# Kernel optimization log

Measured on AMD Instinct MI355X. Metric: run time of the kernel, lower is better.

## Reference

```python
import jax, jax.numpy as jnp
import numpy as np

B, T, E = 4, 2048, 1024
HS = 64            # attention_head_size
NH = E // HS       # num_heads = 16 (all heads share one weight set in the original)


def setup_inputs() -> dict:
    key = jax.random.key(0)
    ks = jax.random.split(key, 6)
    s = 0.02
    x = jax.random.normal(ks[0], (B, T, E), dtype=jnp.float32)
    Wq = jax.random.normal(ks[1], (E, HS), dtype=jnp.float32) * s
    Wk = jax.random.normal(ks[2], (E, HS), dtype=jnp.float32) * s
    Wv = jax.random.normal(ks[3], (E, HS), dtype=jnp.float32) * s
    Wp = jax.random.normal(ks[4], (E, E), dtype=jnp.float32) * s
    bp = jax.random.normal(ks[5], (E,), dtype=jnp.float32) * s
    return {"x": x, "Wq": Wq, "Wk": Wk, "Wv": Wv, "Wp": Wp, "bp": bp}


def reference(x, Wq, Wk, Wv, Wp, bp):
    # Single shared head (the torch module replicates one Head instance NH times).
    hs = Wq.shape[1]
    num_heads = Wp.shape[0] // hs
    q = jnp.einsum('bte,eh->bth', x, Wq)   # [B,T,HS]
    k = jnp.einsum('bte,eh->bth', x, Wk)
    v = jnp.einsum('bte,eh->bth', x, Wv)
    att = jnp.einsum('bqh,bkh->bqk', q, k) * (hs ** -0.5)  # [B,T,T]
    t = x.shape[1]
    causal = jnp.tril(jnp.ones((t, t), dtype=bool))
    att = jnp.where(causal, att, jnp.finfo(att.dtype).min)
    att = jax.nn.softmax(att, axis=-1)
    head = jnp.einsum('bqk,bkh->bqh', att, v)              # [B,T,HS]
    # Concat of identical head outputs == tile along feature dim.
    out = jnp.tile(head, (1, 1, num_heads))                # [B,T,E]
    out = jnp.einsum('bte,ef->btf', out, Wp) + bp          # output projection
    return out
```

## Files before the change

### kernel.cpp

```cpp
#include <hip/hip_runtime.h>
#include <hip/hip_bf16.h>

#define T_SEQ 2048
#define E_DIM 1024
#define HSZ   64
#define NBAT  4
#define QB    64
#define NQT   32

typedef __attribute__((ext_vector_type(8))) short short8;
typedef __attribute__((ext_vector_type(4))) float f32x4;

__device__ inline short f2bf(float f) {
  union { float f; unsigned u; } v; v.f = f;
  unsigned r = v.u + 0x7FFFu + ((v.u >> 16) & 1u);
  return (short)(r >> 16);
}

__global__ __launch_bounds__(256) void wpr_kernel(const float* __restrict__ Wp,
                                                  float* __restrict__ Wpr) {
  int idx = blockIdx.x * 256 + threadIdx.x;
  int f = idx & (E_DIM - 1);
  int j = idx >> 10;
  float s = 0.f;
#pragma unroll
  for (int h = 0; h < 16; ++h) s += Wp[(size_t)(h * HSZ + j) * E_DIM + f];
  Wpr[idx] = s;
}

__global__ __launch_bounds__(256) void wt_kernel(const float* __restrict__ Wq,
    const float* __restrict__ Wk, const float* __restrict__ Wv,
    short* __restrict__ Wt) {
  int idx = blockIdx.x * 256 + threadIdx.x;
  int kk = idx & 63;
  int tmp = idx >> 6;
  int kt = tmp / 192;
  int n = tmp - kt * 192;
  const float* W = (n < 64) ? Wq : (n < 128) ? Wk : Wv;
  Wt[idx] = f2bf(W[(size_t)(kt * 64 + kk) * HSZ + (n & 63)]);
}

__global__ __launch_bounds__(256) void qkv_mfma(const float* __restrict__ X,
    const short* __restrict__ Wt, short* __restrict__ Qo,
    short* __restrict__ Ko, short* __restrict__ Vt) {
  __shared__ short Xs[16 * 64];
  __shared__ short Ws[192 * 64];

  const int tid = threadIdx.x;
  const int m0 = blockIdx.x * 16;
  const int lane = tid & 63, w = tid >> 6;
  const int l15 = lane & 15, l4 = lane >> 4;

  f32x4 acc[3];
  acc[0] = (f32x4)0.f; acc[1] = (f32x4)0.f; acc[2] = (f32x4)0.f;

  for (int kt = 0; kt < 16; ++kt) {
    const int k0 = kt * 64;
    if (tid < 128) {
      int r = tid >> 3, c = tid & 7;
      const float* s = &X[(size_t)(m0 + r) * E_DIM + k0 + c * 8];
      float4 a = *(const float4*)s, d = *(const float4*)(s + 4);
      short8 f;
      f[0] = f2bf(a.x); f[1] = f2bf(a.y); f[2] = f2bf(a.z); f[3] = f2bf(a.w);
      f[4] = f2bf(d.x); f[5] = f2bf(d.y); f[6] = f2bf(d.z); f[7] = f2bf(d.w);
      *(short8*)&Xs[r * 64 + ((c ^ (r & 7)) * 8)] = f;
    }
    {
      const short* wsrc = Wt + (size_t)kt * 12288;
#pragma unroll
      for (int i = 0; i < 6; ++i) {
        int ci = tid + i * 256;
        int r = ci >> 3, c = ci & 7;
        short8 f = *(const short8*)&wsrc[ci * 8];
        *(short8*)&Ws[r * 64 + ((c ^ (r & 7)) * 8)] = f;
      }
    }
    __syncthreads();
#pragma unroll
    for (int ks = 0; ks < 2; ++ks) {
      short8 af = *(short8*)&Xs[l15 * 64 + (((ks * 4 + l4) ^ (l15 & 7)) * 8)];
#pragma unroll
      for (int i = 0; i < 3; ++i) {
        int n = (w * 3 + i) * 16 + l15;
        short8 bf = *(short8*)&Ws[n * 64 + (((ks * 4 + l4) ^ (n & 7)) * 8)];
        acc[i] = __builtin_amdgcn_mfma_f32_16x16x32_bf16(af, bf, acc[i], 0, 0, 0);
      }
    }
    __syncthreads();
  }

  const int b = m0 >> 11, t = m0 & 2047;
#pragma unroll
  for (int i = 0; i < 3; ++i) {
    const int nb = w * 3 + i;
    const int col = (nb & 3) * 16 + l15;
    const int sel = nb >> 2;
#pragma unroll
    for (int reg = 0; reg < 4; ++reg) {
      const int row = l4 * 4 + reg;
      short v = f2bf(acc[i][reg]);
      if (sel == 0)      Qo[(size_t)(m0 + row) * HSZ + col] = v;
      else if (sel == 1) Ko[(size_t)(m0 + row) * HSZ + col] = v;
      else               Vt[((size_t)b * HSZ + col) * T_SEQ + t + row] = v;
    }
  }
}

__global__ __launch_bounds__(256) void attn_part(const short* __restrict__ Q,
    const short* __restrict__ K, const short* __restrict__ Vt,
    float* __restrict__ Opart, float* __restrict__ mpart,
    float* __restrict__ lpart, int splits) {
  const int qt = blockIdx.x;
  const int sp = blockIdx.y;
  const int b  = blockIdx.z;
  const int ntile = qt + 1;
  const int t0 = (sp * ntile) / splits;
  const int t1 = ((sp + 1) * ntile) / splits;
  const int q0 = qt * QB;
  const int pidx = (b * NQT + qt) * splits + sp;
  float* Op = Opart + (size_t)pidx * QB * HSZ;
  float* mp = mpart + (size_t)pidx * QB;
  float* lp = lpart + (size_t)pidx * QB;
  const int tid = threadIdx.x;

  if (t0 >= t1) {
    if (tid < QB) { mp[tid] = -1e30f; lp[tid] = 0.f; }
    return;
  }

  const short* Qb  = Q  + (size_t)b * T_SEQ * HSZ;
  const short* Kb  = K  + (size_t)b * T_SEQ * HSZ;
  const short* Vtb = Vt + (size_t)b * HSZ * T_SEQ;

  __shared__ short Ks[64 * 64];
  __shared__ short Vs[64 * 64];
  __shared__ short Ps[4][16 * 64];

  const int lane = tid & 63;
  const int w    = tid >> 6;
  const int l15  = lane & 15;
  const int l4   = lane >> 4;

  short8 qf[2];
#pragma unroll
  for (int ks = 0; ks < 2; ++ks)
    qf[ks] = *(const short8*)&Qb[(size_t)(q0 + w * 16 + l15) * HSZ + ks * 32 + l4 * 8];

  f32x4 o[4];
  float m_[4], l_[4];
#pragma unroll
  for (int i = 0; i < 4; ++i) { o[i] = (f32x4)0.f; m_[i] = -1e30f; l_[i] = 0.f; }

  for (int kt = t0; kt < t1; ++kt) {
    const int kv0 = kt * 64;
#pragma unroll
    for (int ci = tid; ci < 512; ci += 256) {
      int r = ci >> 3, c = ci & 7;
      short8 f = *(const short8*)&Kb[(size_t)(kv0 + r) * HSZ + c * 8];
      *(short8*)&Ks[r * 64 + ((c ^ (r & 7)) * 8)] = f;
    }
#pragma unroll
    for (int ci = tid; ci < 512; ci += 256) {
      int r = ci >> 3, c = ci & 7;
      short8 f = *(const short8*)&Vtb[(size_t)r * T_SEQ + kv0 + c * 8];
      *(short8*)&Vs[r * 64 + ((c ^ (r & 7)) * 8)] = f;
    }
    __syncthreads();

    f32x4 sacc[4];
#pragma unroll
    for (int nb = 0; nb < 4; ++nb) sacc[nb] = (f32x4)0.f;
#pragma unroll
    for (int nb = 0; nb < 4; ++nb) {
      const int krow = nb * 16 + l15;
#pragma unroll
      for (int ks = 0; ks < 2; ++ks) {
        short8 kf = *(short8*)&Ks[krow * 64 + (((ks * 4 + l4) ^ (krow & 7)) * 8)];
        sacc[nb] = __builtin_amdgcn_mfma_f32_16x16x32_bf16(qf[ks], kf, sacc[nb],
                                                           0, 0, 0);
      }
    }

    const bool diag = (kt == qt);
#pragma unroll
    for (int reg = 0; reg < 4; ++reg) {
      const int grow = q0 + w * 16 + l4 * 4 + reg;
      float sv[4];
      float rmax = -1e30f;
#pragma unroll
      for (int nb = 0; nb < 4; ++nb) {
        sv[nb] = sacc[nb][reg] * 0.125f;
        if (diag && (kv0 + nb * 16 + l15 > grow)) sv[nb] = -1e30f;
        rmax = fmaxf(rmax, sv[nb]);
      }
#pragma unroll
      for (int d = 1; d < 16; d <<= 1) rmax = fmaxf(rmax, __shfl_xor(rmax, d));
      const float mn = fmaxf(m_[reg], rmax);
      const float sc = __expf(m_[reg] - mn);
      float rsum = 0.f;
#pragma unroll
      for (int nb = 0; nb < 4; ++nb) {
        sv[nb] = __expf(sv[nb] - mn);
        rsum += sv[nb];
      }
#pragma unroll
      for (int d = 1; d < 16; d <<= 1) rsum += __shfl_xor(rsum, d);
      l_[reg] = l_[reg] * sc + rsum;
      m_[reg] = mn;
#pragma unroll
      for (int hb = 0; hb < 4; ++hb) o[hb][reg] *= sc;
      const int prow = l4 * 4 + reg;
#pragma unroll
      for (int nb = 0; nb < 4; ++nb) {
        const int col = nb * 16 + l15;
        Ps[w][prow * 64 + (((col >> 3) ^ (prow & 7)) * 8) + (col & 7)] =
            f2bf(sv[nb]);
      }
    }

#pragma unroll
    for (int ks = 0; ks < 2; ++ks) {
      const int prow = l15;
      short8 pf = *(short8*)&Ps[w][prow * 64 + (((ks * 4 + l4) ^ (prow & 7)) * 8)];
#pragma unroll
      for (int hb = 0; hb < 4; ++hb) {
        const int vrow = hb * 16 + l15;
        short8 vf = *(short8*)&Vs[vrow * 64 + (((ks * 4 + l4) ^ (vrow & 7)) * 8)];
        o[hb] = __builtin_amdgcn_mfma_f32_16x16x32_bf16(pf, vf, o[hb], 0, 0, 0);
      }
    }
    __syncthreads();
  }

#pragma unroll
  for (int hb = 0; hb < 4; ++hb)
#pragma unroll
    for (int reg = 0; reg < 4; ++reg)
      Op[(size_t)(w * 16 + l4 * 4 + reg) * HSZ + hb * 16 + l15] = o[hb][reg];
  if (l15 == 0) {
#pragma unroll
    for (int reg = 0; reg < 4; ++reg) {
      mp[w * 16 + l4 * 4 + reg] = m_[reg];
      lp[w * 16 + l4 * 4 + reg] = l_[reg];
    }
  }
}

__global__ __launch_bounds__(256) void attn_combine(
    const float* __restrict__ Opart, const float* __restrict__ mpart,
    const float* __restrict__ lpart, float* __restrict__ Hd, int splits) {
  const int qt = blockIdx.x, b = blockIdx.y;
  const int row = threadIdx.x >> 2;
  const int c0 = (threadIdx.x & 3) * 16;
  const int pbase = (b * NQT + qt) * splits;

  float M = -1e30f;
  for (int s = 0; s < splits; ++s)
    M = fmaxf(M, mpart[(size_t)(pbase + s) * QB + row]);

  float L = 0.f;
  float acc[16];
#pragma unroll
  for (int c = 0; c < 16; ++c) acc[c] = 0.f;

  for (int s = 0; s < splits; ++s) {
    const float ms = mpart[(size_t)(pbase + s) * QB + row];
    const float ls = lpart[(size_t)(pbase + s) * QB + row];
    const float w = __expf(ms - M);
    L += w * ls;
    const float* Op = Opart + ((size_t)(pbase + s) * QB + row) * HSZ + c0;
#pragma unroll
    for (int cc = 0; cc < 16; cc += 4) {
      float4 v = *(const float4*)&Op[cc];
      acc[cc + 0] += w * v.x; acc[cc + 1] += w * v.y;
      acc[cc + 2] += w * v.z; acc[cc + 3] += w * v.w;
    }
  }

  const float inv = 1.f / L;
  float* dst = Hd + ((size_t)b * T_SEQ + qt * QB + row) * HSZ + c0;
#pragma unroll
  for (int cc = 0; cc < 16; cc += 4) {
    float4 v = make_float4(acc[cc] * inv, acc[cc + 1] * inv,
                           acc[cc + 2] * inv, acc[cc + 3] * inv);
    *(float4*)&dst[cc] = v;
  }
}

__global__ __launch_bounds__(256) void proj_kernel(const float* __restrict__ Hd,
    const float* __restrict__ Wpr, const float* __restrict__ bp,
    float* __restrict__ Out) {
  __shared__ float Ht[64][68];
  __shared__ float Ws[64][132];
  const int tid = threadIdx.x;
  const int row0 = blockIdx.x * 64;
  const int c0 = blockIdx.y * 128;

  {
    int c = tid & 15, r0 = tid >> 4;
#pragma unroll
    for (int it = 0; it < 4; ++it) {
      int r = r0 + it * 16;
      float4 hv = *(const float4*)&Hd[(size_t)(row0 + r) * HSZ + c * 4];
      Ht[c * 4 + 0][r] = hv.x; Ht[c * 4 + 1][r] = hv.y;
      Ht[c * 4 + 2][r] = hv.z; Ht[c * 4 + 3][r] = hv.w;
    }
  }
  {
    int c = tid & 31, r0 = tid >> 5;
#pragma unroll
    for (int it = 0; it < 8; ++it) {
      int r = r0 + it * 8;
      *(float4*)&Ws[r][c * 4] =
          *(const float4*)&Wpr[(size_t)r * E_DIM + c0 + c * 4];
    }
  }
  __syncthreads();

  const int tx = tid & 15, ty = tid >> 4;
  float acc[4][8] = {};
#pragma unroll
  for (int k = 0; k < 64; ++k) {
    float4 a = *(const float4*)&Ht[k][ty * 4];
    float4 b0 = *(const float4*)&Ws[k][tx * 8];
    float4 b1 = *(const float4*)&Ws[k][tx * 8 + 4];
    float av[4] = {a.x, a.y, a.z, a.w};
    float bv[8] = {b0.x, b0.y, b0.z, b0.w, b1.x, b1.y, b1.z, b1.w};
#pragma unroll
    for (int i = 0; i < 4; ++i)
#pragma unroll
      for (int j = 0; j < 8; ++j) acc[i][j] += av[i] * bv[j];
  }

#pragma unroll
  for (int i = 0; i < 4; ++i) {
    const int row = row0 + ty * 4 + i;
    float4 v0, v1;
    v0.x = acc[i][0] + bp[c0 + tx * 8 + 0];
    v0.y = acc[i][1] + bp[c0 + tx * 8 + 1];
    v0.z = acc[i][2] + bp[c0 + tx * 8 + 2];
    v0.w = acc[i][3] + bp[c0 + tx * 8 + 3];
    v1.x = acc[i][4] + bp[c0 + tx * 8 + 4];
    v1.y = acc[i][5] + bp[c0 + tx * 8 + 5];
    v1.z = acc[i][6] + bp[c0 + tx * 8 + 6];
    v1.w = acc[i][7] + bp[c0 + tx * 8 + 7];
    *(float4*)&Out[(size_t)row * E_DIM + c0 + tx * 8] = v0;
    *(float4*)&Out[(size_t)row * E_DIM + c0 + tx * 8 + 4] = v1;
  }
}

extern "C" void kernel_launch(void* const* d_in, const int* in_sizes, int n_in,
                              void* d_out, int out_size, void* d_ws,
                              size_t ws_size, hipStream_t stream) {
  (void)in_sizes; (void)n_in; (void)out_size;
  const float* x  = (const float*)d_in[0];
  const float* Wq = (const float*)d_in[1];
  const float* Wk = (const float*)d_in[2];
  const float* Wv = (const float*)d_in[3];
  const float* Wp = (const float*)d_in[4];
  const float* bp = (const float*)d_in[5];
  float* out = (float*)d_out;

  float* ws   = (float*)d_ws;
  short* Qb16 = (short*)(ws);
  short* Kb16 = (short*)(ws + 262144);
  short* Vt16 = (short*)(ws + 524288);
  float* Hd   = ws + 786432;
  float* Wpr  = ws + 1310720;
  short* Wt   = (short*)(ws + 1376256);
  const size_t base = 1474560;

  int splits = 8;
  const size_t per_split = (size_t)NBAT * NQT * (QB * HSZ + 2 * QB);
  while (splits > 1 && (base + per_split * splits) * 4 > ws_size) splits >>= 1;

  float* Opart = ws + base;
  float* mpart = Opart + (size_t)NBAT * NQT * splits * QB * HSZ;
  float* lpart = mpart + (size_t)NBAT * NQT * splits * QB;

  wpr_kernel<<<dim3(256), dim3(256), 0, stream>>>(Wp, Wpr);
  wt_kernel<<<dim3(768), dim3(256), 0, stream>>>(Wq, Wk, Wv, Wt);
  qkv_mfma<<<dim3(512), dim3(256), 0, stream>>>(x, Wt, Qb16, Kb16, Vt16);
  attn_part<<<dim3(NQT, splits, NBAT), dim3(256), 0, stream>>>(
      Qb16, Kb16, Vt16, Opart, mpart, lpart, splits);
  attn_combine<<<dim3(NQT, NBAT), dim3(256), 0, stream>>>(
      Opart, mpart, lpart, Hd, splits);
  proj_kernel<<<dim3(128, 8), dim3(256), 0, stream>>>(Hd, Wpr, bp, out);
}
```

Before: 157.6 us.

## Run output projection on bf16 MFMA with transposed bf16 reduced weights

The output projection moves from an fp32 FMA GEMM staged through shared memory to a bf16 MFMA kernel. It reads the head output and the head-summed projection weights directly from global memory as bf16 fragments. The combine kernel now writes the head output as bf16, and the weight-reduction kernel writes a transposed bf16 copy. This halves intermediate traffic and uses matrix cores, at the cost of bf16 rounding of the head output and weights. The output stores are scalar and strided by row, which may limit write coalescing.

New measurement: 150.3 us. 4.7% less time.

```diff
diff --git a/kernel.cpp b/kernel.cpp
--- a/kernel.cpp
+++ b/kernel.cpp
@@ -18,14 +18,14 @@
 }
 
 __global__ __launch_bounds__(256) void wpr_kernel(const float* __restrict__ Wp,
-                                                  float* __restrict__ Wpr) {
+                                                  short* __restrict__ Wpb) {
   int idx = blockIdx.x * 256 + threadIdx.x;
   int f = idx & (E_DIM - 1);
   int j = idx >> 10;
   float s = 0.f;
 #pragma unroll
   for (int h = 0; h < 16; ++h) s += Wp[(size_t)(h * HSZ + j) * E_DIM + f];
-  Wpr[idx] = s;
+  Wpb[(size_t)f * HSZ + j] = f2bf(s);
 }
 
 __global__ __launch_bounds__(256) void wt_kernel(const float* __restrict__ Wq,
@@ -248,7 +248,7 @@
 
 __global__ __launch_bounds__(256) void attn_combine(
     const float* __restrict__ Opart, const float* __restrict__ mpart,
-    const float* __restrict__ lpart, float* __restrict__ Hd, int splits) {
+    const float* __restrict__ lpart, short* __restrict__ Hd16, int splits) {
   const int qt = blockIdx.x, b = blockIdx.y;
   const int row = threadIdx.x >> 2;
   const int c0 = (threadIdx.x & 3) * 16;
@@ -278,74 +278,43 @@
   }
 
   const float inv = 1.f / L;
-  float* dst = Hd + ((size_t)b * T_SEQ + qt * QB + row) * HSZ + c0;
-#pragma unroll
-  for (int cc = 0; cc < 16; cc += 4) {
-    float4 v = make_float4(acc[cc] * inv, acc[cc + 1] * inv,
-                           acc[cc + 2] * inv, acc[cc + 3] * inv);
-    *(float4*)&dst[cc] = v;
-  }
-}
-
-__global__ __launch_bounds__(256) void proj_kernel(const float* __restrict__ Hd,
-    const float* __restrict__ Wpr, const float* __restrict__ bp,
+  short* dst = Hd16 + ((size_t)b * T_SEQ + qt * QB + row) * HSZ + c0;
+  short8 v0, v1;
+#pragma unroll
+  for (int cc = 0; cc < 8; ++cc) {
+    v0[cc] = f2bf(acc[cc] * inv);
+    v1[cc] = f2bf(acc[8 + cc] * inv);
+  }
+  *(short8*)dst = v0;
+  *(short8*)(dst + 8) = v1;
+}
+
+__global__ __launch_bounds__(256) void proj_mfma(const short* __restrict__ Hd16,
+    const short* __restrict__ Wpb, const float* __restrict__ bp,
     float* __restrict__ Out) {
-  __shared__ float Ht[64][68];
-  __shared__ float Ws[64][132];
   const int tid = threadIdx.x;
-  const int row0 = blockIdx.x * 64;
-  const int c0 = blockIdx.y * 128;
-
-  {
-    int c = tid & 15, r0 = tid >> 4;
-#pragma unroll
-    for (int it = 0; it < 4; ++it) {
-      int r = r0 + it * 16;
-      float4 hv = *(const float4*)&Hd[(size_t)(row0 + r) * HSZ + c * 4];
-      Ht[c * 4 + 0][r] = hv.x; Ht[c * 4 + 1][r] = hv.y;
-      Ht[c * 4 + 2][r] = hv.z; Ht[c * 4 + 3][r] = hv.w;
-    }
-  }
-  {
-    int c = tid & 31, r0 = tid >> 5;
-#pragma unroll
-    for (int it = 0; it < 8; ++it) {
-      int r = r0 + it * 8;
-      *(float4*)&Ws[r][c * 4] =
-          *(const float4*)&Wpr[(size_t)r * E_DIM + c0 + c * 4];
-    }
-  }
-  __syncthreads();
-
-  const int tx = tid & 15, ty = tid >> 4;
-  float acc[4][8] = {};
-#pragma unroll
-  for (int k = 0; k < 64; ++k) {
-    float4 a = *(const float4*)&Ht[k][ty * 4];
-    float4 b0 = *(const float4*)&Ws[k][tx * 8];
-    float4 b1 = *(const float4*)&Ws[k][tx * 8 + 4];
-    float av[4] = {a.x, a.y, a.z, a.w};
-    float bv[8] = {b0.x, b0.y, b0.z, b0.w, b1.x, b1.y, b1.z, b1.w};
-#pragma unroll
-    for (int i = 0; i < 4; ++i)
-#pragma unroll
-      for (int j = 0; j < 8; ++j) acc[i][j] += av[i] * bv[j];
-  }
-
-#pragma unroll
-  for (int i = 0; i < 4; ++i) {
-    const int row = row0 + ty * 4 + i;
-    float4 v0, v1;
-    v0.x = acc[i][0] + bp[c0 + tx * 8 + 0];
-    v0.y = acc[i][1] + bp[c0 + tx * 8 + 1];
-    v0.z = acc[i][2] + bp[c0 + tx * 8 + 2];
-    v0.w = acc[i][3] + bp[c0 + tx * 8 + 3];
-    v1.x = acc[i][4] + bp[c0 + tx * 8 + 4];
-    v1.y = acc[i][5] + bp[c0 + tx * 8 + 5];
-    v1.z = acc[i][6] + bp[c0 + tx * 8 + 6];
-    v1.w = acc[i][7] + bp[c0 + tx * 8 + 7];
-    *(float4*)&Out[(size_t)row * E_DIM + c0 + tx * 8] = v0;
-    *(float4*)&Out[(size_t)row * E_DIM + c0 + tx * 8 + 4] = v1;
+  const int lane = tid & 63, w = tid >> 6;
+  const int l15 = lane & 15, l4 = lane >> 4;
+  const int m0 = blockIdx.x * 64 + w * 16;
+  const int n0 = blockIdx.y * 128;
+
+  const short* asrc = &Hd16[(size_t)(m0 + l15) * HSZ + l4 * 8];
+  short8 af0 = *(const short8*)asrc;
+  short8 af1 = *(const short8*)(asrc + 32);
+
+#pragma unroll
+  for (int nb = 0; nb < 8; ++nb) {
+    const int n = n0 + nb * 16 + l15;
+    const short* bsrc = &Wpb[(size_t)n * HSZ + l4 * 8];
+    short8 b0 = *(const short8*)bsrc;
+    short8 b1 = *(const short8*)(bsrc + 32);
+    f32x4 acc = (f32x4)0.f;
+    acc = __builtin_amdgcn_mfma_f32_16x16x32_bf16(af0, b0, acc, 0, 0, 0);
+    acc = __builtin_amdgcn_mfma_f32_16x16x32_bf16(af1, b1, acc, 0, 0, 0);
+    const float bpv = bp[n];
+#pragma unroll
+    for (int reg = 0; reg < 4; ++reg)
+      Out[(size_t)(m0 + l4 * 4 + reg) * E_DIM + n] = acc[reg] + bpv;
   }
 }
 
@@ -365,10 +334,10 @@
   short* Qb16 = (short*)(ws);
   short* Kb16 = (short*)(ws + 262144);
   short* Vt16 = (short*)(ws + 524288);
-  float* Hd   = ws + 786432;
-  float* Wpr  = ws + 1310720;
-  short* Wt   = (short*)(ws + 1376256);
-  const size_t base = 1474560;
+  short* Hd16 = (short*)(ws + 786432);
+  short* Wpb  = (short*)(ws + 1048576);
+  short* Wt   = (short*)(ws + 1081344);
+  const size_t base = 1179648;
 
   int splits = 8;
   const size_t per_split = (size_t)NBAT * NQT * (QB * HSZ + 2 * QB);
@@ -378,12 +347,12 @@
   float* mpart = Opart + (size_t)NBAT * NQT * splits * QB * HSZ;
   float* lpart = mpart + (size_t)NBAT * NQT * splits * QB;
 
-  wpr_kernel<<<dim3(256), dim3(256), 0, stream>>>(Wp, Wpr);
+  wpr_kernel<<<dim3(256), dim3(256), 0, stream>>>(Wp, Wpb);
   wt_kernel<<<dim3(768), dim3(256), 0, stream>>>(Wq, Wk, Wv, Wt);
   qkv_mfma<<<dim3(512), dim3(256), 0, stream>>>(x, Wt, Qb16, Kb16, Vt16);
   attn_part<<<dim3(NQT, splits, NBAT), dim3(256), 0, stream>>>(
       Qb16, Kb16, Vt16, Opart, mpart, lpart, splits);
   attn_combine<<<dim3(NQT, NBAT), dim3(256), 0, stream>>>(
-      Opart, mpart, lpart, Hd, splits);
-  proj_kernel<<<dim3(128, 8), dim3(256), 0, stream>>>(Hd, Wpr, bp, out);
-}
+      Opart, mpart, lpart, Hd16, splits);
+  proj_mfma<<<dim3(128, 8), dim3(256), 0, stream>>>(Hd16, Wpb, bp, out);
+}
```
